# Performance work log

Measured on AMD Instinct MI355X. Metric: run time of the kernel, lower is better.

The kernel has to match this reference:

```python
import jax, jax.numpy as jnp
import numpy as np

V_MIN = -10.0
V_MAX = 10.0
NUM_ATOMS = 51
ATOM_DELTA = (V_MAX - V_MIN) / (NUM_ATOMS - 1)
BS = 1_000_000


def setup_inputs() -> dict:
    key = jax.random.key(0)
    k1, k2 = jax.random.split(key)
    reward = jax.random.normal(k1, (BS,), dtype=jnp.float32) * 3.0
    probs = jax.random.uniform(k2, (BS, NUM_ATOMS), dtype=jnp.float32)
    atom_values = (V_MIN + ATOM_DELTA * jnp.arange(NUM_ATOMS)).astype(jnp.float32)
    return {"reward": reward, "probs": probs, "atom_values": atom_values}


def reference(reward, probs, atom_values):
    # Categorical (C51) Bellman projection, expressed as a scatter-add
    # instead of the original's dense [bs, A, A] projection matrix + bmm.
    bs, A = probs.shape
    # shifted & clamped atom support: [bs, A]
    new_vals = jnp.clip(atom_values[None, :] + reward[:, None], V_MIN, V_MAX)
    idx = (new_vals - V_MIN) / ATOM_DELTA           # fractional atom index
    lower = jnp.floor(idx)
    upper = jnp.ceil(idx)
    same = lower == upper                           # idx landed exactly on an atom
    l_coef = jnp.where(same, 1.0, upper - idx)      # original sets 1.0 when l == u
    u_coef = idx - lower                            # 0 when same
    li = lower.astype(jnp.int32)
    ui = upper.astype(jnp.int32)
    rows = jnp.broadcast_to(jnp.arange(bs)[:, None], (bs, A))
    out = jnp.zeros_like(probs)
    out = out.at[rows, li].add(l_coef * probs)
    out = out.at[rows, ui].add(u_coef * probs)
    return out
```

## Files before the change

### kernel.cpp

```cpp
#include <hip/hip_runtime.h>

#define NA 51
#define TPB 256
#define RPW 16
#define RPB 64
#define KCLAMP 52

typedef float v4u __attribute__((ext_vector_type(4), aligned(4)));
typedef float v2u __attribute__((ext_vector_type(2), aligned(4)));
typedef float v4a __attribute__((ext_vector_type(4), aligned(16)));

__global__ __launch_bounds__(TPB, 8) void c51_bellman_kernel(
    const float* __restrict__ reward,
    const float* __restrict__ probs,
    float* __restrict__ out,
    int bs)
{
    __shared__ __align__(16) float lds[4][RPW * NA];
    const int tid  = threadIdx.x;
    const int lane = tid & 63;
    const int wv   = tid >> 6;
    const int q    = lane & 3;
    const int lr   = lane >> 2;
    const int wrow0 = blockIdx.x * RPB + wv * RPW;
    const int r     = wrow0 + lr;
    const bool edge = (blockIdx.x == 0) | (blockIdx.x == (int)gridDim.x - 1);

    float* const wlds = lds[wv];
    const int a0    = 13 * q;
    const int count = (q < 3) ? 13 : 12;

    if (r < bs) {
        const float s  = reward[r] * 2.5f;
        const float kf = floorf(s);
        const float f  = s - kf;
        int k = (int)kf;
        k = min(max(k, -KCLAMP), KCLAMP);
        const float* rp = probs + (size_t)r * NA;

        float row[13];
        *(v4u*)&row[0] = *(const v4u*)&rp[a0];
        *(v4u*)&row[4] = *(const v4u*)&rp[a0 + 4];
        *(v4u*)&row[8] = *(const v4u*)&rp[a0 + 8];
        row[12] = (q < 3) ? rp[a0 + 12] : 0.0f;

        float w[14];
        if (!edge) {
            const float* wb = rp + a0 - k - 1;
            *(v4u*)&w[0]  = *(const v4u*)&wb[0];
            *(v4u*)&w[4]  = *(const v4u*)&wb[4];
            *(v4u*)&w[8]  = *(const v4u*)&wb[8];
            *(v2u*)&w[12] = *(const v2u*)&wb[12];
        } else {
            #pragma unroll
            for (int m = 0; m < 14; ++m)
                w[m] = rp[min(max(a0 + m - k - 1, 0), NA - 1)];
        }

        float m_lo = 0.0f, m_hi = 0.0f;
        #pragma unroll
        for (int c = 0; c < 13; ++c) {
            const float t = (float)(a0 + c) + s;
            if (t < 0.0f)  m_lo += row[c];
            if (t > 50.0f) m_hi += row[c];
        }
        m_lo += __shfl_xor(m_lo, 1, 64); m_lo += __shfl_xor(m_lo, 2, 64);
        m_hi += __shfl_xor(m_hi, 1, 64); m_hi += __shfl_xor(m_hi, 2, 64);

        const float w1 = 1.0f - f;
        float* wp = wlds + lr * NA + a0;
        #pragma unroll
        for (int c = 0; c < 13; ++c) {
            const int i = a0 + c;
            const float pl = ((unsigned)(i - k - 1) <= 50u) ? w[c]     : 0.0f;
            const float cu = ((unsigned)(i - k)     <= 50u) ? w[c + 1] : 0.0f;
            float o;
            if (i == 0)           o = w1 * cu + m_lo;
            else if (i == NA - 1) o = ((f == 0.0f) ? cu : f * pl) + m_hi;
            else                  o = w1 * cu + f * pl;
            if (c < count) wp[c] = o;
        }
    }

    const int nrw   = min(RPW, max(0, bs - wrow0));
    const int nelem = nrw * NA;
    const int n4    = nelem >> 2;
    const v4a* l4 = (const v4a*)wlds;
    v4a* o4 = (v4a*)(out + (size_t)wrow0 * NA);
    for (int e = lane; e < n4; e += 64) o4[e] = l4[e];
    for (int e = (n4 << 2) + lane; e < nelem; e += 64)
        out[(size_t)wrow0 * NA + e] = wlds[e];
}

extern "C" void kernel_launch(void* const* d_in, const int* in_sizes, int n_in,
                              void* d_out, int out_size, void* d_ws, size_t ws_size,
                              hipStream_t stream) {
    const float* reward = (const float*)d_in[0];
    const float* probs  = (const float*)d_in[1];
    float* out = (float*)d_out;
    const int bs = in_sizes[0];

    const int blocks = (bs + RPB - 1) / RPB;
    c51_bellman_kernel<<<blocks, TPB, 0, stream>>>(reward, probs, out, bs);
}
```

Before: 341.2 us.

## Stage probs rows into LDS via direct global-to-LDS loads and compute in place

Each wave now copies its 16 contiguous probs rows straight into LDS with fully coalesced 16-byte global_load_lds transfers. It then does the shifted-window reads and the projection from LDS instead of issuing unaligned per-lane global loads. Guard padding around the LDS buffer plus the existing index masks replace the clamped edge path, and results are written in place before the coalesced store to global. The aim is to cut inefficient scattered global traffic, at the cost of a full vmcnt wait and extra LDS reads.

```diff
diff --git a/kernel.cpp b/kernel.cpp
--- a/kernel.cpp
+++ b/kernel.cpp
@@ -4,11 +4,14 @@
 #define TPB 256
 #define RPW 16
 #define RPB 64
+#define WNF (RPW * NA)
+#define GUARD 56
 #define KCLAMP 52
 
-typedef float v4u __attribute__((ext_vector_type(4), aligned(4)));
-typedef float v2u __attribute__((ext_vector_type(2), aligned(4)));
 typedef float v4a __attribute__((ext_vector_type(4), aligned(16)));
+
+#define WAITV0 do { asm volatile("s_waitcnt vmcnt(0)" ::: "memory"); \
+                    __builtin_amdgcn_sched_barrier(0); } while (0)
 
 __global__ __launch_bounds__(TPB, 8) void c51_bellman_kernel(
     const float* __restrict__ reward,
@@ -16,46 +19,60 @@
     float* __restrict__ out,
     int bs)
 {
-    __shared__ __align__(16) float lds[4][RPW * NA];
+    __shared__ __align__(16) float lds[GUARD + 4 * WNF + GUARD];
     const int tid  = threadIdx.x;
     const int lane = tid & 63;
     const int wv   = tid >> 6;
     const int q    = lane & 3;
     const int lr   = lane >> 2;
     const int wrow0 = blockIdx.x * RPB + wv * RPW;
-    const int r     = wrow0 + lr;
-    const bool edge = (blockIdx.x == 0) | (blockIdx.x == (int)gridDim.x - 1);
 
-    float* const wlds = lds[wv];
-    const int a0    = 13 * q;
-    const int count = (q < 3) ? 13 : 12;
+    float* const wb = lds + GUARD + wv * WNF;
+    const int nrw  = min(RPW, max(0, bs - wrow0));
+    const bool full = (nrw == RPW);
 
-    if (r < bs) {
-        const float s  = reward[r] * 2.5f;
+    if (full) {
+        const char* src = (const char*)(probs + (size_t)wrow0 * NA);
+        #pragma unroll
+        for (int c = 0; c < 3; ++c) {
+            __builtin_amdgcn_global_load_lds(
+                (const __attribute__((address_space(1))) void*)
+                    (unsigned long long)(src + c * 1024 + lane * 16),
+                (__attribute__((address_space(3))) void*)
+                    (unsigned long long)(wb + c * 256),
+                16, 0, 0);
+        }
+        if (lane < 12) {
+            __builtin_amdgcn_global_load_lds(
+                (const __attribute__((address_space(1))) void*)
+                    (unsigned long long)(src + 3072 + lane * 16),
+                (__attribute__((address_space(3))) void*)
+                    (unsigned long long)(wb + 768),
+                16, 0, 0);
+        }
+    } else if (nrw > 0) {
+        const int ne = nrw * NA;
+        for (int e = lane; e < ne; e += 64)
+            wb[e] = probs[(size_t)wrow0 * NA + e];
+    }
+
+    float s = 0.0f;
+    if (lr < nrw) s = reward[wrow0 + lr] * 2.5f;
+    WAITV0;
+
+    if (lr < nrw) {
         const float kf = floorf(s);
         const float f  = s - kf;
         int k = (int)kf;
         k = min(max(k, -KCLAMP), KCLAMP);
-        const float* rp = probs + (size_t)r * NA;
+        float* const rp = wb + lr * NA;
+        const int a0    = 13 * q;
+        const int count = (q < 3) ? 13 : 12;
 
         float row[13];
-        *(v4u*)&row[0] = *(const v4u*)&rp[a0];
-        *(v4u*)&row[4] = *(const v4u*)&rp[a0 + 4];
-        *(v4u*)&row[8] = *(const v4u*)&rp[a0 + 8];
+        #pragma unroll
+        for (int c = 0; c < 12; ++c) row[c] = rp[a0 + c];
         row[12] = (q < 3) ? rp[a0 + 12] : 0.0f;
-
-        float w[14];
-        if (!edge) {
-            const float* wb = rp + a0 - k - 1;
-            *(v4u*)&w[0]  = *(const v4u*)&wb[0];
-            *(v4u*)&w[4]  = *(const v4u*)&wb[4];
-            *(v4u*)&w[8]  = *(const v4u*)&wb[8];
-            *(v2u*)&w[12] = *(const v2u*)&wb[12];
-        } else {
-            #pragma unroll
-            for (int m = 0; m < 14; ++m)
-                w[m] = rp[min(max(a0 + m - k - 1, 0), NA - 1)];
-        }
 
         float m_lo = 0.0f, m_hi = 0.0f;
         #pragma unroll
@@ -67,8 +84,13 @@
         m_lo += __shfl_xor(m_lo, 1, 64); m_lo += __shfl_xor(m_lo, 2, 64);
         m_hi += __shfl_xor(m_hi, 1, 64); m_hi += __shfl_xor(m_hi, 2, 64);
 
+        float w[14];
+        const float* wsrc = rp + a0 - k - 1;
+        #pragma unroll
+        for (int m = 0; m < 14; ++m) w[m] = wsrc[m];
+
         const float w1 = 1.0f - f;
-        float* wp = wlds + lr * NA + a0;
+        float* wp = rp + a0;
         #pragma unroll
         for (int c = 0; c < 13; ++c) {
             const int i = a0 + c;
@@ -82,14 +104,13 @@
         }
     }
 
-    const int nrw   = min(RPW, max(0, bs - wrow0));
-    const int nelem = nrw * NA;
-    const int n4    = nelem >> 2;
-    const v4a* l4 = (const v4a*)wlds;
+    const int ne = nrw * NA;
+    const int n4 = ne >> 2;
+    const v4a* l4 = (const v4a*)wb;
     v4a* o4 = (v4a*)(out + (size_t)wrow0 * NA);
     for (int e = lane; e < n4; e += 64) o4[e] = l4[e];
-    for (int e = (n4 << 2) + lane; e < nelem; e += 64)
-        out[(size_t)wrow0 * NA + e] = wlds[e];
+    for (int e = (n4 << 2) + lane; e < ne; e += 64)
+        out[(size_t)wrow0 * NA + e] = wb[e];
 }
 
 extern "C" void kernel_launch(void* const* d_in, const int* in_sizes, int n_in,
```

New measurement: 343.2 us. About the same (+0.6%).
